# Optimization experiments

Measured on AMD Instinct MI355X. Metric: run time of the kernel, lower is better.

The kernel has to match this reference:

```python
import jax, jax.numpy as jnp
import numpy as np

# --- static config (matches init_kwargs / input_specs) ---
N_GRAPHS = 32
NODES = 1000          # num_nodes per graph
N = N_GRAPHS * NODES  # 32000 total nodes
F_IN = 128            # num_features
E_DIM = 16            # edge_attr_dim
H, C = 4, 16          # heads, GAT_dim
HC = H * C            # 64
E = 512000            # edges (before self-loops)
PROJ = 8              # proj_nodes
OUT = 256             # output_dim
NEG_SLOPE = 0.2       # PyG GATConv default


def setup_inputs() -> dict:
    key = jax.random.key(0)
    ks = jax.random.split(key, 20)
    s = 0.1
    return {
        "x": jax.random.normal(ks[0], (N, F_IN), jnp.float32),
        "edge_attr": jax.random.normal(ks[1], (E, E_DIM), jnp.float32),
        # layer 0 (input_conv): F_IN -> H*C
        "W0":   jax.random.normal(ks[2], (F_IN, HC), jnp.float32) * s,
        "a_s0": jax.random.normal(ks[3], (H, C), jnp.float32) * s,
        "a_d0": jax.random.normal(ks[4], (H, C), jnp.float32) * s,
        "W_e0": jax.random.normal(ks[5], (E_DIM, HC), jnp.float32) * s,
        "a_e0": jax.random.normal(ks[6], (H, C), jnp.float32) * s,
        "b0":   jnp.zeros((HC,), jnp.float32),
        # layers 1..2 stacked: HC -> H*C
        "Wg":   jax.random.normal(ks[7], (2, HC, HC), jnp.float32) * s,
        "a_sg": jax.random.normal(ks[8], (2, H, C), jnp.float32) * s,
        "a_dg": jax.random.normal(ks[9], (2, H, C), jnp.float32) * s,
        "W_eg": jax.random.normal(ks[10], (2, E_DIM, HC), jnp.float32) * s,
        "a_eg": jax.random.normal(ks[11], (2, H, C), jnp.float32) * s,
        "bg":   jnp.zeros((2, HC), jnp.float32),
        # node_proj: HC -> PROJ ; fc_out: NODES*PROJ -> OUT
        "Wp": jax.random.normal(ks[12], (HC, PROJ), jnp.float32) * s,
        "bp": jnp.zeros((PROJ,), jnp.float32),
        "Wo": jax.random.normal(ks[13], (NODES * PROJ, OUT), jnp.float32) * (s / 4),
        "bo": jnp.zeros((OUT,), jnp.float32),
        "edge_index": jax.random.randint(ks[14], (2, E), 0, N, jnp.int32),
        "batch": jnp.repeat(jnp.arange(N_GRAPHS, dtype=jnp.int32), NODES),
    }


def _gat_layer(x, src, dst, eattr, W, a_s, a_d, W_e, a_e, b):
    """PyG GATConv (concat=True, shared src/dst lin, edge_dim) forward."""
    xl = (x @ W).reshape(N, H, C)                       # [N,H,C]
    al_s = jnp.sum(xl * a_s, axis=-1)                   # [N,H]
    al_d = jnp.sum(xl * a_d, axis=-1)                   # [N,H]
    el = (eattr @ W_e).reshape(-1, H, C)                # [Ef,H,C]
    al_e = jnp.sum(el * a_e, axis=-1)                   # [Ef,H]
    logits = jax.nn.leaky_relu(al_s[src] + al_d[dst] + al_e, NEG_SLOPE)
    # segment softmax over destination nodes (every node has a self-loop)
    mx = jax.ops.segment_max(logits, dst, num_segments=N)
    p = jnp.exp(logits - mx[dst])
    denom = jax.ops.segment_sum(p, dst, num_segments=N)
    alpha = p / denom[dst]                               # [Ef,H]
    out = jax.ops.segment_sum(xl[src] * alpha[..., None], dst, num_segments=N)
    return out.reshape(N, HC) + b


def reference(x, edge_attr, W0, a_s0, a_d0, W_e0, a_e0, b0,
              Wg, a_sg, a_dg, W_eg, a_eg, bg,
              Wp, bp, Wo, bo, edge_index, batch):
    src, dst = edge_index[0], edge_index[1]
    # PyG add_self_loops with fill_value='mean': per-dst mean of incoming edge_attr
    deg = jax.ops.segment_sum(jnp.ones((E,), edge_attr.dtype), dst, num_segments=N)
    loop_attr = jax.ops.segment_sum(edge_attr, dst, num_segments=N) / jnp.maximum(deg, 1.0)[:, None]
    loops = jnp.arange(N, dtype=src.dtype)
    src_f = jnp.concatenate([src, loops])
    dst_f = jnp.concatenate([dst, loops])
    ea_f = jnp.concatenate([edge_attr, loop_attr], axis=0)   # [E+N, E_DIM]

    h = jax.nn.relu(_gat_layer(x, src_f, dst_f, ea_f, W0, a_s0, a_d0, W_e0, a_e0, b0))
    for i in range(2):
        h = jax.nn.relu(_gat_layer(h, src_f, dst_f, ea_f,
                                   Wg[i], a_sg[i], a_dg[i], W_eg[i], a_eg[i], bg[i]))
    h = jax.nn.relu(h @ Wp + bp)                             # [N, PROJ]
    B = batch.shape[0] // NODES                              # static batch count
    h = h.reshape(B, NODES * PROJ)
    return h @ Wo + bo                                       # [B, OUT]
```

## Files before the change

kernel.cpp:

```cpp
#include <hip/hip_runtime.h>
#include <hip/hip_bf16.h>
#include <hip/hip_fp16.h>

#define N_NODES 32000
#define FIN     128
#define E_EDGES 512000
#define EF_EDGES 544000
#define HC      64
#define XSTR    72
#define NGRAPH  32
#define PROJ    8
#define OUT_DIM 256

static __device__ inline unsigned short f2bf(float f) {
  unsigned int x = __float_as_uint(f);
  unsigned int r = (x + 0x7fffu + ((x >> 16) & 1u)) >> 16;
  return (unsigned short)r;
}
static __device__ inline float bf2f(unsigned short u) {
  return __uint_as_float((unsigned int)u << 16);
}
static __device__ inline unsigned short f2h(float f) {
  return __half_as_ushort(__float2half(f));
}
static __device__ inline float h2f(unsigned short u) {
  return __half2float(__ushort_as_half(u));
}

__global__ __launch_bounds__(256) void zero_kernel(int* __restrict__ deg) {
  deg[blockIdx.x * 256 + threadIdx.x] = 0;
}

__global__ __launch_bounds__(256) void deg_kernel(const int* __restrict__ ei,
                                                  int* __restrict__ deg) {
  int e = blockIdx.x * 256 + threadIdx.x;
  atomicAdd(&deg[ei[E_EDGES + e]], 1);
}

__global__ __launch_bounds__(256) void scan1_kernel(const int* __restrict__ deg,
                                                    int* __restrict__ offs,
                                                    int* __restrict__ bsum) {
  int idx = blockIdx.x * 256 + threadIdx.x;
  int lane = threadIdx.x & 63;
  int w = threadIdx.x >> 6;
  int v = deg[idx] + 1;
  int s = v;
#pragma unroll
  for (int off = 1; off < 64; off <<= 1) {
    int t = __shfl_up(s, off);
    if (lane >= off) s += t;
  }
  __shared__ int wsum[4];
  if (lane == 63) wsum[w] = s;
  __syncthreads();
  int add = 0;
#pragma unroll
  for (int i = 0; i < 4; ++i) add += (i < w) ? wsum[i] : 0;
  int incl = s + add;
  offs[idx] = incl - v;
  if (threadIdx.x == 255) bsum[blockIdx.x] = incl;
}

__global__ __launch_bounds__(256) void scan3_kernel(const int* __restrict__ bsum,
                                                    int* __restrict__ offs,
                                                    int* __restrict__ nxt) {
  __shared__ int wsum[4];
  int tid = threadIdx.x, bid = blockIdx.x;
  int lane = tid & 63, w = tid >> 6;
  int v = (tid < bid) ? bsum[tid] : 0;
#pragma unroll
  for (int off = 1; off < 64; off <<= 1) v += __shfl_xor(v, off);
  if (lane == 0) wsum[w] = v;
  __syncthreads();
  int boff = wsum[0] + wsum[1] + wsum[2] + wsum[3];
  int idx = bid * 256 + tid;
  int o = offs[idx] + boff;
  offs[idx] = o;
  nxt[idx] = o;
  if (bid == 0 && tid == 0) offs[N_NODES] = EF_EDGES;
}

__global__ __launch_bounds__(256) void fill_kernel(const int* __restrict__ ei,
                                                   int* __restrict__ nxt,
                                                   int* __restrict__ csr_src,
                                                   int* __restrict__ csr_eid) {
  int e = blockIdx.x * 256 + threadIdx.x;
  int s, d;
  if (e < E_EDGES) { s = ei[e]; d = ei[E_EDGES + e]; }
  else             { s = e - E_EDGES; d = s; }
  int pos = atomicAdd(&nxt[d], 1);
  csr_src[pos] = s;
  csr_eid[pos] = e;
}

__device__ __forceinline__ void compute_Me(float (*sMe)[16][4],
                                           const float* __restrict__ W_e0,
                                           const float* __restrict__ a_e0,
                                           const float* __restrict__ W_eg,
                                           const float* __restrict__ a_eg) {
  int tid = threadIdx.x;
  if (tid < 192) {
    int l = tid >> 6, r6 = tid & 63, d = r6 >> 2, h = r6 & 3;
    const float* We = (l == 0) ? W_e0 : W_eg + (size_t)(l - 1) * 16 * HC;
    const float* ae = (l == 0) ? a_e0 : a_eg + (size_t)(l - 1) * 64;
    float s = 0.f;
#pragma unroll
    for (int c = 0; c < 16; ++c) s += We[d * HC + h * 16 + c] * ae[h * 16 + c];
    sMe[l][d][h] = s;
  }
  __syncthreads();
}

__global__ __launch_bounds__(256) void edge_kernel(const float* __restrict__ edge_attr,
                                                   const float* __restrict__ W_e0,
                                                   const float* __restrict__ a_e0,
                                                   const float* __restrict__ W_eg,
                                                   const float* __restrict__ a_eg,
                                                   const int* __restrict__ offs,
                                                   const int* __restrict__ csr_eid,
                                                   unsigned short* __restrict__ lgE) {
  __shared__ float sMe[3][16][4];
  __shared__ float sMean[4][16];
  compute_Me(sMe, W_e0, a_e0, W_eg, a_eg);
  int b = blockIdx.x;
  int tid = threadIdx.x;
  if (b < 8000) {
    int lane = tid & 63, wv = tid >> 6;
    int n = b * 4 + wv;
    int k = lane & 15, g = lane >> 4;
    int beg = offs[n], end = offs[n + 1];
    float s = 0.f;
    int posl = -1;
    for (int i = beg + g; i < end; i += 4) {
      int e = csr_eid[i];
      if (e < E_EDGES) s += edge_attr[(size_t)e * 16 + k];
      else posl = i;
    }
    s += __shfl_xor(s, 16);
    s += __shfl_xor(s, 32);
    posl = max(posl, __shfl_xor(posl, 16));
    posl = max(posl, __shfl_xor(posl, 32));
    int degv = end - beg - 1;
    float mean = s / fmaxf((float)degv, 1.f);
    if (g == 0) sMean[wv][k] = mean;
    if (lane < 3) {
      int l = lane;
      float r0 = 0.f, r1 = 0.f, r2 = 0.f, r3 = 0.f;
#pragma unroll
      for (int d = 0; d < 16; ++d) {
        float a = sMean[wv][d];
        r0 = fmaf(a, sMe[l][d][0], r0);
        r1 = fmaf(a, sMe[l][d][1], r1);
        r2 = fmaf(a, sMe[l][d][2], r2);
        r3 = fmaf(a, sMe[l][d][3], r3);
      }
      unsigned long long u =
          (unsigned long long)f2h(r0) |
          ((unsigned long long)f2h(r1) << 16) |
          ((unsigned long long)f2h(r2) << 32) |
          ((unsigned long long)f2h(r3) << 48);
      *(unsigned long long*)&lgE[((size_t)l * EF_EDGES + posl) * 4] = u;
    }
  } else {
    int pos = (b - 8000) * 256 + tid;
    int e = csr_eid[pos];
    if (e < E_EDGES) {
      float av[16];
      *(float4*)&av[0]  = *(const float4*)&edge_attr[(size_t)e * 16 + 0];
      *(float4*)&av[4]  = *(const float4*)&edge_attr[(size_t)e * 16 + 4];
      *(float4*)&av[8]  = *(const float4*)&edge_attr[(size_t)e * 16 + 8];
      *(float4*)&av[12] = *(const float4*)&edge_attr[(size_t)e * 16 + 12];
#pragma unroll
      for (int l = 0; l < 3; ++l) {
        float r0 = 0.f, r1 = 0.f, r2 = 0.f, r3 = 0.f;
#pragma unroll
        for (int d = 0; d < 16; ++d) {
          float a = av[d];
          r0 = fmaf(a, sMe[l][d][0], r0);
          r1 = fmaf(a, sMe[l][d][1], r1);
          r2 = fmaf(a, sMe[l][d][2], r2);
          r3 = fmaf(a, sMe[l][d][3], r3);
        }
        unsigned long long u =
            (unsigned long long)f2h(r0) |
            ((unsigned long long)f2h(r1) << 16) |
            ((unsigned long long)f2h(r2) << 32) |
            ((unsigned long long)f2h(r3) << 48);
        __builtin_nontemporal_store(
            u, (unsigned long long*)&lgE[((size_t)l * EF_EDGES + pos) * 4]);
      }
    }
  }
}

template <int K>
__global__ __launch_bounds__(256) void transform_kernel(const float* __restrict__ A,
                                                        const float* __restrict__ W,
                                                        const float* __restrict__ a_s,
                                                        const float* __restrict__ a_d,
                                                        unsigned short* __restrict__ xlb,
                                                        float* __restrict__ al_d) {
  __shared__ float sW[64][64];
  __shared__ float sA[64][65];
  int tid = threadIdx.x;
  int row0 = blockIdx.x * 64;
  int tx = tid & 15, ty = tid >> 4;
  int c0 = tx * 4, r0 = ty * 4;
  float acc[4][4] = {};
  for (int kc = 0; kc < K; kc += 64) {
    for (int i = tid; i < 1024; i += 256) {
      int kk = i >> 4, c4 = (i & 15) * 4;
      *(float4*)&sW[kk][c4] = *(const float4*)&W[(size_t)(kc + kk) * HC + c4];
    }
    for (int i = tid; i < 1024; i += 256) {
      int r = i >> 4, k4 = (i & 15) * 4;
      float4 v = *(const float4*)&A[(size_t)(row0 + r) * K + kc + k4];
      sA[r][k4 + 0] = v.x; sA[r][k4 + 1] = v.y;
      sA[r][k4 + 2] = v.z; sA[r][k4 + 3] = v.w;
    }
    __syncthreads();
#pragma unroll 8
    for (int kk = 0; kk < 64; ++kk) {
      float4 w = *(float4*)&sW[kk][c0];
      float a0 = sA[r0 + 0][kk];
      float a1 = sA[r0 + 1][kk];
      float a2 = sA[r0 + 2][kk];
      float a3 = sA[r0 + 3][kk];
      acc[0][0] = fmaf(a0, w.x, acc[0][0]); acc[0][1] = fmaf(a0, w.y, acc[0][1]);
      acc[0][2] = fmaf(a0, w.z, acc[0][2]); acc[0][3] = fmaf(a0, w.w, acc[0][3]);
      acc[1][0] = fmaf(a1, w.x, acc[1][0]); acc[1][1] = fmaf(a1, w.y, acc[1][1]);
      acc[1][2] = fmaf(a1, w.z, acc[1][2]); acc[1][3] = fmaf(a1, w.w, acc[1][3]);
      acc[2][0] = fmaf(a2, w.x, acc[2][0]); acc[2][1] = fmaf(a2, w.y, acc[2][1]);
      acc[2][2] = fmaf(a2, w.z, acc[2][2]); acc[2][3] = fmaf(a2, w.w, acc[2][3]);
      acc[3][0] = fmaf(a3, w.x, acc[3][0]); acc[3][1] = fmaf(a3, w.y, acc[3][1]);
      acc[3][2] = fmaf(a3, w.z, acc[3][2]); acc[3][3] = fmaf(a3, w.w, acc[3][3]);
    }
    __syncthreads();
  }
  float asv[4], adv[4];
#pragma unroll
  for (int j = 0; j < 4; ++j) { asv[j] = a_s[c0 + j]; adv[j] = a_d[c0 + j]; }
  int hd = tx >> 2;
#pragma unroll
  for (int i = 0; i < 4; ++i) {
    int r = row0 + r0 + i;
    ushort4 u = make_ushort4(f2bf(acc[i][0]), f2bf(acc[i][1]),
                             f2bf(acc[i][2]), f2bf(acc[i][3]));
    *(ushort4*)&xlb[(size_t)r * XSTR + c0] = u;
    float ps = acc[i][0] * asv[0] + acc[i][1] * asv[1] + acc[i][2] * asv[2] + acc[i][3] * asv[3];
    float pd = acc[i][0] * adv[0] + acc[i][1] * adv[1] + acc[i][2] * adv[2] + acc[i][3] * adv[3];
    ps += __shfl_xor(ps, 1); ps += __shfl_xor(ps, 2);
    pd += __shfl_xor(pd, 1); pd += __shfl_xor(pd, 2);
    if ((tx & 3) == 0) {
      *(float*)&xlb[(size_t)r * XSTR + 64 + hd * 2] = ps;
      al_d[(size_t)r * 4 + hd] = pd;
    }
  }
}

template <int FUSE_PROJ>
__global__ __launch_bounds__(256, 4) void gather_kernel(const int* __restrict__ offs,
                                                        const int* __restrict__ csr_src,
                                                        const unsigned short* __restrict__ lg,
                                                        const unsigned short* __restrict__ xlb,
                                                        const float* __restrict__ al_d,
                                                        const float* __restrict__ bias,
                                                        const float* __restrict__ Wp,
                                                        const float* __restrict__ bp,
                                                        float* __restrict__ outp) {
  int tid = threadIdx.x;
  int lane = tid & 63;
  int n = blockIdx.x * 4 + (tid >> 6);
  int u = lane & 31;
  int hf = lane >> 5;
  int c0 = u * 2;
  int hd = u >> 3;
  int beg = offs[n], end = offs[n + 1];
  float ald = al_d[(size_t)n * 4 + hd];
  float denom = 0.f, a0 = 0.f, a1 = 0.f;
  for (int ib = beg; ib < end; ib += 16) {
    int sq[8]; unsigned short gq[8]; float pm[8];
#pragma unroll
    for (int q = 0; q < 8; ++q) {
      int j = ib + hf + q * 2;
      bool ok = j < end;
      int jc = ok ? j : beg;
      sq[q] = csr_src[jc];
      gq[q] = lg[(size_t)jc * 4 + hd];
      pm[q] = ok ? 1.f : 0.f;
    }
    unsigned int xq[8]; float alsq[8];
#pragma unroll
    for (int q = 0; q < 8; ++q) {
      const unsigned short* row = &xlb[(size_t)sq[q] * XSTR];
      xq[q] = *(const unsigned int*)&row[c0];
      alsq[q] = *(const float*)&row[64 + hd * 2];
    }
#pragma unroll
    for (int q = 0; q < 8; ++q) {
      float l = h2f(gq[q]) + alsq[q] + ald;
      l = (l > 0.f) ? l : 0.2f * l;
      float p = pm[q] * __expf(l);
      denom += p;
      a0 = fmaf(p, bf2f((unsigned short)(xq[q] & 0xffff)), a0);
      a1 = fmaf(p, bf2f((unsigned short)(xq[q] >> 16)), a1);
    }
  }
  denom += __shfl_xor(denom, 32);
  a0 += __shfl_xor(a0, 32);
  a1 += __shfl_xor(a1, 32);
  float hv0 = fmaxf(a0 / denom + bias[c0], 0.f);
  float hv1 = fmaxf(a1 / denom + bias[c0 + 1], 0.f);
  if constexpr (!FUSE_PROJ) {
    if (hf == 0) {
      float2 o; o.x = hv0; o.y = hv1;
      *(float2*)&outp[(size_t)n * HC + c0] = o;
    }
  } else {
    float pj[8];
#pragma unroll
    for (int j = 0; j < 8; ++j)
      pj[j] = (hf == 0) ? hv0 * Wp[c0 * PROJ + j] + hv1 * Wp[(c0 + 1) * PROJ + j] : 0.f;
#pragma unroll
    for (int off = 1; off < 64; off <<= 1) {
#pragma unroll
      for (int j = 0; j < 8; ++j) pj[j] += __shfl_xor(pj[j], off);
    }
    if (lane < 8) {
      float v = pj[0];
      v = (lane == 1) ? pj[1] : v;
      v = (lane == 2) ? pj[2] : v;
      v = (lane == 3) ? pj[3] : v;
      v = (lane == 4) ? pj[4] : v;
      v = (lane == 5) ? pj[5] : v;
      v = (lane == 6) ? pj[6] : v;
      v = (lane == 7) ? pj[7] : v;
      outp[(size_t)n * PROJ + lane] = fmaxf(v + bp[lane], 0.f);
    }
  }
}

__global__ __launch_bounds__(256) void fc1_kernel(const float* __restrict__ p,
                                                  const float* __restrict__ Wo,
                                                  float* __restrict__ part) {
  __shared__ float sp[NGRAPH][250];
  int kc = blockIdx.x;
  int ct = blockIdx.y;
  int tid = threadIdx.x;
  for (int i = tid; i < NGRAPH * 250; i += 256) {
    int g = i / 250, kk = i % 250;
    sp[g][kk] = p[(size_t)g * 8000 + kc * 250 + kk];
  }
  __syncthreads();
  int c = ct * 64 + (tid & 63);
  int kg = tid >> 6;
  float acc[NGRAPH] = {};
  for (int kk = kg; kk < 250; kk += 4) {
    float w = __builtin_nontemporal_load(&Wo[(size_t)(kc * 250 + kk) * OUT_DIM + c]);
#pragma unroll
    for (int g = 0; g < NGRAPH; ++g) acc[g] = fmaf(sp[g][kk], w, acc[g]);
  }
  int ch = kc * 4 + kg;
#pragma unroll
  for (int g = 0; g < NGRAPH; ++g)
    part[((size_t)ch * NGRAPH + g) * OUT_DIM + c] = acc[g];
}

__global__ __launch_bounds__(256) void fc2_kernel(const float* __restrict__ part,
                                                  const float* __restrict__ bo,
                                                  float* __restrict__ out) {
  int i = blockIdx.x * 256 + threadIdx.x;
  int g = i >> 8, c = i & 255;
  float s = bo[c];
  for (int ch = 0; ch < 128; ++ch) s += part[((size_t)ch * NGRAPH + g) * OUT_DIM + c];
  out[i] = s;
}

extern "C" void kernel_launch(void* const* d_in, const int* in_sizes, int n_in,
                              void* d_out, int out_size, void* d_ws, size_t ws_size,
                              hipStream_t stream) {
  const float* x         = (const float*)d_in[0];
  const float* edge_attr = (const float*)d_in[1];
  const float* W0        = (const float*)d_in[2];
  const float* a_s0      = (const float*)d_in[3];
  const float* a_d0      = (const float*)d_in[4];
  const float* W_e0      = (const float*)d_in[5];
  const float* a_e0      = (const float*)d_in[6];
  const float* b0        = (const float*)d_in[7];
  const float* Wg        = (const float*)d_in[8];
  const float* a_sg      = (const float*)d_in[9];
  const float* a_dg      = (const float*)d_in[10];
  const float* W_eg      = (const float*)d_in[11];
  const float* a_eg      = (const float*)d_in[12];
  const float* bg        = (const float*)d_in[13];
  const float* Wp        = (const float*)d_in[14];
  const float* bp        = (const float*)d_in[15];
  const float* Wo        = (const float*)d_in[16];
  const float* bo        = (const float*)d_in[17];
  const int*   ei        = (const int*)d_in[18];

  char* base = (char*)d_ws;
  size_t off = 0;
  auto alloc = [&](size_t bytes) -> void* {
    void* ptr = base + off;
    off = (off + bytes + 255) & ~(size_t)255;
    return ptr;
  };
  int*            deg     = (int*)alloc((size_t)N_NODES * 4);
  int*            offs    = (int*)alloc((size_t)(N_NODES + 1) * 4);
  int*            nxt     = (int*)alloc((size_t)N_NODES * 4);
  int*            bsum    = (int*)alloc(128 * 4);
  int*            csr_src = (int*)alloc((size_t)EF_EDGES * 4);
  int*            csr_eid = (int*)alloc((size_t)EF_EDGES * 4);
  unsigned short* lgE     = (unsigned short*)alloc((size_t)3 * EF_EDGES * 4 * 2);
  unsigned short* xlb     = (unsigned short*)alloc((size_t)N_NODES * XSTR * 2);
  float*          al_d    = (float*)alloc((size_t)N_NODES * 4 * 4);
  float*          hA      = (float*)alloc((size_t)N_NODES * HC * 4);
  float*          hB      = (float*)alloc((size_t)N_NODES * HC * 4);
  float*          pbuf    = (float*)alloc((size_t)N_NODES * PROJ * 4);
  float*          part    = (float*)alloc((size_t)128 * NGRAPH * OUT_DIM * 4);

  zero_kernel<<<N_NODES / 256, 256, 0, stream>>>(deg);
  deg_kernel<<<E_EDGES / 256, 256, 0, stream>>>(ei, deg);
  scan1_kernel<<<N_NODES / 256, 256, 0, stream>>>(deg, offs, bsum);
  scan3_kernel<<<N_NODES / 256, 256, 0, stream>>>(bsum, offs, nxt);
  fill_kernel<<<EF_EDGES / 256, 256, 0, stream>>>(ei, nxt, csr_src, csr_eid);
  edge_kernel<<<8000 + 2125, 256, 0, stream>>>(edge_attr, W_e0, a_e0, W_eg, a_eg,
                                               offs, csr_eid, lgE);
  transform_kernel<FIN><<<N_NODES / 64, 256, 0, stream>>>(x, W0, a_s0, a_d0, xlb, al_d);

  gather_kernel<0><<<N_NODES / 4, 256, 0, stream>>>(offs, csr_src, lgE, xlb,
                                                    al_d, b0, Wp, bp, hA);
  transform_kernel<HC><<<N_NODES / 64, 256, 0, stream>>>(hA, Wg, a_sg, a_dg, xlb, al_d);
  gather_kernel<0><<<N_NODES / 4, 256, 0, stream>>>(offs, csr_src, lgE + (size_t)EF_EDGES * 4,
                                                    xlb, al_d, bg, Wp, bp, hB);
  transform_kernel<HC><<<N_NODES / 64, 256, 0, stream>>>(hB, Wg + HC * HC, a_sg + 64,
                                                         a_dg + 64, xlb, al_d);
  gather_kernel<1><<<N_NODES / 4, 256, 0, stream>>>(offs, csr_src, lgE + (size_t)2 * EF_EDGES * 4,
                                                    xlb, al_d, bg + 64, Wp, bp, pbuf);

  fc1_kernel<<<dim3(32, 4), 256, 0, stream>>>(pbuf, Wo, part);
  fc2_kernel<<<NGRAPH, 256, 0, stream>>>(part, bo, (float*)d_out);
}
```

Measured before the change: 274.7 us.

## Split node features and edge logits into head halves for gather locality

Node features, source attention scalars and edge logits are stored in two head-half planes (heads 0-1 and heads 2-3). The gather kernel now launches two blocks per four nodes, one per half, so each wave's random-row working set is half as large and more of it can stay in cache. The projection partials from the two halves are summed in fc1, which now also applies the projection bias and relu. The cost is twice as many gather blocks, with the csr_src index loads repeated per half.

```diff
diff --git a/kernel.cpp b/kernel.cpp
--- a/kernel.cpp
+++ b/kernel.cpp
@@ -7,7 +7,6 @@
 #define E_EDGES 512000
 #define EF_EDGES 544000
 #define HC      64
-#define XSTR    72
 #define NGRAPH  32
 #define PROJ    8
 #define OUT_DIM 256
@@ -118,7 +117,7 @@
                                                    const float* __restrict__ a_eg,
                                                    const int* __restrict__ offs,
                                                    const int* __restrict__ csr_eid,
-                                                   unsigned short* __restrict__ lgE) {
+                                                   unsigned short* __restrict__ lgEH) {
   __shared__ float sMe[3][16][4];
   __shared__ float sMean[4][16];
   compute_Me(sMe, W_e0, a_e0, W_eg, a_eg);
@@ -143,23 +142,17 @@
     int degv = end - beg - 1;
     float mean = s / fmaxf((float)degv, 1.f);
     if (g == 0) sMean[wv][k] = mean;
-    if (lane < 3) {
-      int l = lane;
-      float r0 = 0.f, r1 = 0.f, r2 = 0.f, r3 = 0.f;
+    if (lane < 6) {
+      int l = lane >> 1, half = lane & 1;
+      float ra = 0.f, rb = 0.f;
 #pragma unroll
       for (int d = 0; d < 16; ++d) {
         float a = sMean[wv][d];
-        r0 = fmaf(a, sMe[l][d][0], r0);
-        r1 = fmaf(a, sMe[l][d][1], r1);
-        r2 = fmaf(a, sMe[l][d][2], r2);
-        r3 = fmaf(a, sMe[l][d][3], r3);
+        ra = fmaf(a, sMe[l][d][half * 2 + 0], ra);
+        rb = fmaf(a, sMe[l][d][half * 2 + 1], rb);
       }
-      unsigned long long u =
-          (unsigned long long)f2h(r0) |
-          ((unsigned long long)f2h(r1) << 16) |
-          ((unsigned long long)f2h(r2) << 32) |
-          ((unsigned long long)f2h(r3) << 48);
-      *(unsigned long long*)&lgE[((size_t)l * EF_EDGES + posl) * 4] = u;
+      unsigned int u = (unsigned int)f2h(ra) | ((unsigned int)f2h(rb) << 16);
+      *(unsigned int*)&lgEH[(((size_t)l * 2 + half) * EF_EDGES + posl) * 2] = u;
     }
   } else {
     int pos = (b - 8000) * 256 + tid;
@@ -181,13 +174,12 @@
           r2 = fmaf(a, sMe[l][d][2], r2);
           r3 = fmaf(a, sMe[l][d][3], r3);
         }
-        unsigned long long u =
-            (unsigned long long)f2h(r0) |
-            ((unsigned long long)f2h(r1) << 16) |
-            ((unsigned long long)f2h(r2) << 32) |
-            ((unsigned long long)f2h(r3) << 48);
+        unsigned int u0 = (unsigned int)f2h(r0) | ((unsigned int)f2h(r1) << 16);
+        unsigned int u1 = (unsigned int)f2h(r2) | ((unsigned int)f2h(r3) << 16);
         __builtin_nontemporal_store(
-            u, (unsigned long long*)&lgE[((size_t)l * EF_EDGES + pos) * 4]);
+            u0, (unsigned int*)&lgEH[(((size_t)l * 2 + 0) * EF_EDGES + pos) * 2]);
+        __builtin_nontemporal_store(
+            u1, (unsigned int*)&lgEH[(((size_t)l * 2 + 1) * EF_EDGES + pos) * 2]);
       }
     }
   }
@@ -198,7 +190,8 @@
                                                         const float* __restrict__ W,
                                                         const float* __restrict__ a_s,
                                                         const float* __restrict__ a_d,
-                                                        unsigned short* __restrict__ xlb,
+                                                        unsigned short* __restrict__ xlbH,
+                                                        float* __restrict__ al_sh,
                                                         float* __restrict__ al_d) {
   __shared__ float sW[64][64];
   __shared__ float sA[64][65];
@@ -241,63 +234,69 @@
 #pragma unroll
   for (int j = 0; j < 4; ++j) { asv[j] = a_s[c0 + j]; adv[j] = a_d[c0 + j]; }
   int hd = tx >> 2;
+  int half = c0 >> 5, cih = c0 & 31;
 #pragma unroll
   for (int i = 0; i < 4; ++i) {
     int r = row0 + r0 + i;
     ushort4 u = make_ushort4(f2bf(acc[i][0]), f2bf(acc[i][1]),
                              f2bf(acc[i][2]), f2bf(acc[i][3]));
-    *(ushort4*)&xlb[(size_t)r * XSTR + c0] = u;
+    *(ushort4*)&xlbH[((size_t)half * N_NODES + r) * 32 + cih] = u;
     float ps = acc[i][0] * asv[0] + acc[i][1] * asv[1] + acc[i][2] * asv[2] + acc[i][3] * asv[3];
     float pd = acc[i][0] * adv[0] + acc[i][1] * adv[1] + acc[i][2] * adv[2] + acc[i][3] * adv[3];
     ps += __shfl_xor(ps, 1); ps += __shfl_xor(ps, 2);
     pd += __shfl_xor(pd, 1); pd += __shfl_xor(pd, 2);
     if ((tx & 3) == 0) {
-      *(float*)&xlb[(size_t)r * XSTR + 64 + hd * 2] = ps;
+      al_sh[((size_t)(hd >> 1) * N_NODES + r) * 2 + (hd & 1)] = ps;
       al_d[(size_t)r * 4 + hd] = pd;
     }
   }
 }
 
 template <int FUSE_PROJ>
-__global__ __launch_bounds__(256, 4) void gather_kernel(const int* __restrict__ offs,
-                                                        const int* __restrict__ csr_src,
-                                                        const unsigned short* __restrict__ lg,
-                                                        const unsigned short* __restrict__ xlb,
-                                                        const float* __restrict__ al_d,
-                                                        const float* __restrict__ bias,
-                                                        const float* __restrict__ Wp,
-                                                        const float* __restrict__ bp,
-                                                        float* __restrict__ outp) {
+__global__ __launch_bounds__(256) void gather_kernel(const int* __restrict__ offs,
+                                                     const int* __restrict__ csr_src,
+                                                     const unsigned short* __restrict__ lgL,
+                                                     const unsigned short* __restrict__ xlbH,
+                                                     const float* __restrict__ al_sh,
+                                                     const float* __restrict__ al_d,
+                                                     const float* __restrict__ bias,
+                                                     const float* __restrict__ Wp,
+                                                     const float* __restrict__ bp,
+                                                     float* __restrict__ outp) {
   int tid = threadIdx.x;
+  int bid = blockIdx.x;
+  int half = bid & 1;
+  int n = (bid >> 1) * 4 + (tid >> 6);
   int lane = tid & 63;
-  int n = blockIdx.x * 4 + (tid >> 6);
-  int u = lane & 31;
-  int hf = lane >> 5;
-  int c0 = u * 2;
-  int hd = u >> 3;
+  int u16 = lane & 15;
+  int gr = lane >> 4;
+  int c0 = u16 * 2;
+  int hd = u16 >> 3;
+  const unsigned short* lgH = lgL + (size_t)half * EF_EDGES * 2;
+  const unsigned short* xh  = xlbH + (size_t)half * N_NODES * 32;
+  const float* ash          = al_sh + (size_t)half * N_NODES * 2;
   int beg = offs[n], end = offs[n + 1];
-  float ald = al_d[(size_t)n * 4 + hd];
+  float ald = al_d[(size_t)n * 4 + half * 2 + hd];
   float denom = 0.f, a0 = 0.f, a1 = 0.f;
-  for (int ib = beg; ib < end; ib += 16) {
-    int sq[8]; unsigned short gq[8]; float pm[8];
-#pragma unroll
-    for (int q = 0; q < 8; ++q) {
-      int j = ib + hf + q * 2;
+  for (int jb = beg; jb < end; jb += 16) {
+    int sq[4]; unsigned short gq[4]; float pm[4];
+#pragma unroll
+    for (int q = 0; q < 4; ++q) {
+      int j = jb + gr + q * 4;
       bool ok = j < end;
       int jc = ok ? j : beg;
       sq[q] = csr_src[jc];
-      gq[q] = lg[(size_t)jc * 4 + hd];
+      gq[q] = lgH[(size_t)jc * 2 + hd];
       pm[q] = ok ? 1.f : 0.f;
     }
-    unsigned int xq[8]; float alsq[8];
-#pragma unroll
-    for (int q = 0; q < 8; ++q) {
-      const unsigned short* row = &xlb[(size_t)sq[q] * XSTR];
-      xq[q] = *(const unsigned int*)&row[c0];
-      alsq[q] = *(const float*)&row[64 + hd * 2];
-    }
-#pragma unroll
-    for (int q = 0; q < 8; ++q) {
+    unsigned int xq[4]; float alsq[4];
+#pragma unroll
+    for (int q = 0; q < 4; ++q) {
+      xq[q] = *(const unsigned int*)&xh[(size_t)sq[q] * 32 + c0];
+      alsq[q] = ash[(size_t)sq[q] * 2 + hd];
+    }
+#pragma unroll
+    for (int q = 0; q < 4; ++q) {
       float l = h2f(gq[q]) + alsq[q] + ald;
       l = (l > 0.f) ? l : 0.2f * l;
       float p = pm[q] * __expf(l);
@@ -306,21 +305,22 @@
       a1 = fmaf(p, bf2f((unsigned short)(xq[q] >> 16)), a1);
     }
   }
-  denom += __shfl_xor(denom, 32);
-  a0 += __shfl_xor(a0, 32);
-  a1 += __shfl_xor(a1, 32);
-  float hv0 = fmaxf(a0 / denom + bias[c0], 0.f);
-  float hv1 = fmaxf(a1 / denom + bias[c0 + 1], 0.f);
+  denom += __shfl_xor(denom, 16); denom += __shfl_xor(denom, 32);
+  a0 += __shfl_xor(a0, 16); a0 += __shfl_xor(a0, 32);
+  a1 += __shfl_xor(a1, 16); a1 += __shfl_xor(a1, 32);
+  int gc = half * 32 + c0;
+  float hv0 = fmaxf(a0 / denom + bias[gc], 0.f);
+  float hv1 = fmaxf(a1 / denom + bias[gc + 1], 0.f);
   if constexpr (!FUSE_PROJ) {
-    if (hf == 0) {
+    if (gr == 0) {
       float2 o; o.x = hv0; o.y = hv1;
-      *(float2*)&outp[(size_t)n * HC + c0] = o;
+      *(float2*)&outp[(size_t)n * HC + gc] = o;
     }
   } else {
     float pj[8];
 #pragma unroll
     for (int j = 0; j < 8; ++j)
-      pj[j] = (hf == 0) ? hv0 * Wp[c0 * PROJ + j] + hv1 * Wp[(c0 + 1) * PROJ + j] : 0.f;
+      pj[j] = (gr == 0) ? hv0 * Wp[gc * PROJ + j] + hv1 * Wp[(gc + 1) * PROJ + j] : 0.f;
 #pragma unroll
     for (int off = 1; off < 64; off <<= 1) {
 #pragma unroll
@@ -335,21 +335,24 @@
       v = (lane == 5) ? pj[5] : v;
       v = (lane == 6) ? pj[6] : v;
       v = (lane == 7) ? pj[7] : v;
-      outp[(size_t)n * PROJ + lane] = fmaxf(v + bp[lane], 0.f);
-    }
-  }
-}
-
-__global__ __launch_bounds__(256) void fc1_kernel(const float* __restrict__ p,
+      outp[((size_t)half * N_NODES + n) * PROJ + lane] = v;
+    }
+  }
+}
+
+__global__ __launch_bounds__(256) void fc1_kernel(const float* __restrict__ pH,
+                                                  const float* __restrict__ bp,
                                                   const float* __restrict__ Wo,
                                                   float* __restrict__ part) {
   __shared__ float sp[NGRAPH][250];
   int kc = blockIdx.x;
   int ct = blockIdx.y;
   int tid = threadIdx.x;
+  const float* pH1 = pH + (size_t)N_NODES * PROJ;
   for (int i = tid; i < NGRAPH * 250; i += 256) {
     int g = i / 250, kk = i % 250;
-    sp[g][kk] = p[(size_t)g * 8000 + kc * 250 + kk];
+    size_t flat = (size_t)g * 8000 + kc * 250 + kk;
+    sp[g][kk] = fmaxf(pH[flat] + pH1[flat] + bp[flat & 7], 0.f);
   }
   __syncthreads();
   int c = ct * 64 + (tid & 63);
@@ -412,12 +415,13 @@
   int*            bsum    = (int*)alloc(128 * 4);
   int*            csr_src = (int*)alloc((size_t)EF_EDGES * 4);
   int*            csr_eid = (int*)alloc((size_t)EF_EDGES * 4);
-  unsigned short* lgE     = (unsigned short*)alloc((size_t)3 * EF_EDGES * 4 * 2);
-  unsigned short* xlb     = (unsigned short*)alloc((size_t)N_NODES * XSTR * 2);
+  unsigned short* lgEH    = (unsigned short*)alloc((size_t)6 * EF_EDGES * 2 * 2);
+  unsigned short* xlbH    = (unsigned short*)alloc((size_t)2 * N_NODES * 32 * 2);
+  float*          al_sh   = (float*)alloc((size_t)2 * N_NODES * 2 * 4);
   float*          al_d    = (float*)alloc((size_t)N_NODES * 4 * 4);
   float*          hA      = (float*)alloc((size_t)N_NODES * HC * 4);
   float*          hB      = (float*)alloc((size_t)N_NODES * HC * 4);
-  float*          pbuf    = (float*)alloc((size_t)N_NODES * PROJ * 4);
+  float*          pbufH   = (float*)alloc((size_t)2 * N_NODES * PROJ * 4);
   float*          part    = (float*)alloc((size_t)128 * NGRAPH * OUT_DIM * 4);
 
   zero_kernel<<<N_NODES / 256, 256, 0, stream>>>(deg);
@@ -426,19 +430,21 @@
   scan3_kernel<<<N_NODES / 256, 256, 0, stream>>>(bsum, offs, nxt);
   fill_kernel<<<EF_EDGES / 256, 256, 0, stream>>>(ei, nxt, csr_src, csr_eid);
   edge_kernel<<<8000 + 2125, 256, 0, stream>>>(edge_attr, W_e0, a_e0, W_eg, a_eg,
-                                               offs, csr_eid, lgE);
-  transform_kernel<FIN><<<N_NODES / 64, 256, 0, stream>>>(x, W0, a_s0, a_d0, xlb, al_d);
-
-  gather_kernel<0><<<N_NODES / 4, 256, 0, stream>>>(offs, csr_src, lgE, xlb,
-                                                    al_d, b0, Wp, bp, hA);
-  transform_kernel<HC><<<N_NODES / 64, 256, 0, stream>>>(hA, Wg, a_sg, a_dg, xlb, al_d);
-  gather_kernel<0><<<N_NODES / 4, 256, 0, stream>>>(offs, csr_src, lgE + (size_t)EF_EDGES * 4,
-                                                    xlb, al_d, bg, Wp, bp, hB);
+                                               offs, csr_eid, lgEH);
+  transform_kernel<FIN><<<N_NODES / 64, 256, 0, stream>>>(x, W0, a_s0, a_d0,
+                                                          xlbH, al_sh, al_d);
+
+  gather_kernel<0><<<16000, 256, 0, stream>>>(offs, csr_src, lgEH, xlbH,
+                                              al_sh, al_d, b0, Wp, bp, hA);
+  transform_kernel<HC><<<N_NODES / 64, 256, 0, stream>>>(hA, Wg, a_sg, a_dg,
+                                                         xlbH, al_sh, al_d);
+  gather_kernel<0><<<16000, 256, 0, stream>>>(offs, csr_src, lgEH + (size_t)2 * EF_EDGES * 2,
+                                              xlbH, al_sh, al_d, bg, Wp, bp, hB);
   transform_kernel<HC><<<N_NODES / 64, 256, 0, stream>>>(hB, Wg + HC * HC, a_sg + 64,
-                                                         a_dg + 64, xlb, al_d);
-  gather_kernel<1><<<N_NODES / 4, 256, 0, stream>>>(offs, csr_src, lgE + (size_t)2 * EF_EDGES * 4,
-                                                    xlb, al_d, bg + 64, Wp, bp, pbuf);
-
-  fc1_kernel<<<dim3(32, 4), 256, 0, stream>>>(pbuf, Wo, part);
+                                                         a_dg + 64, xlbH, al_sh, al_d);
+  gather_kernel<1><<<16000, 256, 0, stream>>>(offs, csr_src, lgEH + (size_t)4 * EF_EDGES * 2,
+                                              xlbH, al_sh, al_d, bg + 64, Wp, bp, pbufH);
+
+  fc1_kernel<<<dim3(32, 4), 256, 0, stream>>>(pbufH, bp, Wo, part);
   fc2_kernel<<<NGRAPH, 256, 0, stream>>>(part, bo, (float*)d_out);
 }
```

Result: slower. 299.6 us (+9.1%).

## Compute edge attention logits once per edge-head and broadcast via shuffles

Applied to the files above, without the earlier changes.

The gather kernel used to compute each edge's attention logit and exp redundantly in all 8 lanes that share a head. It now assigns one lane per (edge, head) pair for 16 edges at a time, so exp and the logit loads happen once. The probabilities and source indices are then broadcast with wave shuffles to the lanes that accumulate the feature columns. The exchange costs many extra shuffles per batch of edges, and the launch-bounds occupancy hint is dropped.

```diff
diff --git a/kernel.cpp b/kernel.cpp
--- a/kernel.cpp
+++ b/kernel.cpp
@@ -259,60 +259,58 @@
 }
 
 template <int FUSE_PROJ>
-__global__ __launch_bounds__(256, 4) void gather_kernel(const int* __restrict__ offs,
-                                                        const int* __restrict__ csr_src,
-                                                        const unsigned short* __restrict__ lg,
-                                                        const unsigned short* __restrict__ xlb,
-                                                        const float* __restrict__ al_d,
-                                                        const float* __restrict__ bias,
-                                                        const float* __restrict__ Wp,
-                                                        const float* __restrict__ bp,
-                                                        float* __restrict__ outp) {
+__global__ __launch_bounds__(256) void gather_kernel(const int* __restrict__ offs,
+                                                     const int* __restrict__ csr_src,
+                                                     const unsigned short* __restrict__ lg,
+                                                     const unsigned short* __restrict__ xlb,
+                                                     const float* __restrict__ al_d,
+                                                     const float* __restrict__ bias,
+                                                     const float* __restrict__ Wp,
+                                                     const float* __restrict__ bp,
+                                                     float* __restrict__ outp) {
   int tid = threadIdx.x;
   int lane = tid & 63;
   int n = blockIdx.x * 4 + (tid >> 6);
-  int u = lane & 31;
-  int hf = lane >> 5;
-  int c0 = u * 2;
-  int hd = u >> 3;
+  int q16 = lane >> 2, hd4 = lane & 3;
+  int eu = lane >> 5, v = lane & 31;
+  int hdB = v >> 3;
   int beg = offs[n], end = offs[n + 1];
-  float ald = al_d[(size_t)n * 4 + hd];
-  float denom = 0.f, a0 = 0.f, a1 = 0.f;
-  for (int ib = beg; ib < end; ib += 16) {
-    int sq[8]; unsigned short gq[8]; float pm[8];
-#pragma unroll
-    for (int q = 0; q < 8; ++q) {
-      int j = ib + hf + q * 2;
-      bool ok = j < end;
-      int jc = ok ? j : beg;
-      sq[q] = csr_src[jc];
-      gq[q] = lg[(size_t)jc * 4 + hd];
-      pm[q] = ok ? 1.f : 0.f;
-    }
-    unsigned int xq[8]; float alsq[8];
-#pragma unroll
-    for (int q = 0; q < 8; ++q) {
-      const unsigned short* row = &xlb[(size_t)sq[q] * XSTR];
-      xq[q] = *(const unsigned int*)&row[c0];
-      alsq[q] = *(const float*)&row[64 + hd * 2];
-    }
-#pragma unroll
-    for (int q = 0; q < 8; ++q) {
-      float l = h2f(gq[q]) + alsq[q] + ald;
-      l = (l > 0.f) ? l : 0.2f * l;
-      float p = pm[q] * __expf(l);
-      denom += p;
-      a0 = fmaf(p, bf2f((unsigned short)(xq[q] & 0xffff)), a0);
-      a1 = fmaf(p, bf2f((unsigned short)(xq[q] >> 16)), a1);
-    }
-  }
-  denom += __shfl_xor(denom, 32);
+  float ald = al_d[(size_t)n * 4 + hd4];
+  float denq = 0.f, a0 = 0.f, a1 = 0.f;
+  for (int jb = beg; jb < end; jb += 16) {
+    int j = jb + q16;
+    bool ok = j < end;
+    int jc = ok ? j : beg;
+    int sq = csr_src[jc];
+    unsigned short lgv = lg[(size_t)jc * 4 + hd4];
+    const unsigned short* rowA = &xlb[(size_t)sq * XSTR];
+    float als = *(const float*)&rowA[64 + hd4 * 2];
+    float l = h2f(lgv) + als + ald;
+    l = fmaxf(l, 0.2f * l);
+    float p = ok ? __expf(l) : 0.f;
+    denq += p;
+#pragma unroll
+    for (int k = 0; k < 8; ++k) {
+      int e = k * 2 + eu;
+      int se = __shfl(sq, e * 4);
+      float pe = __shfl(p, e * 4 + hdB);
+      unsigned int xx = *(const unsigned int*)&xlb[(size_t)se * XSTR + 2 * v];
+      a0 = fmaf(pe, bf2f((unsigned short)(xx & 0xffff)), a0);
+      a1 = fmaf(pe, bf2f((unsigned short)(xx >> 16)), a1);
+    }
+  }
+  denq += __shfl_xor(denq, 4);
+  denq += __shfl_xor(denq, 8);
+  denq += __shfl_xor(denq, 16);
+  denq += __shfl_xor(denq, 32);
+  float denom = __shfl(denq, hdB);
   a0 += __shfl_xor(a0, 32);
   a1 += __shfl_xor(a1, 32);
+  int c0 = v * 2;
   float hv0 = fmaxf(a0 / denom + bias[c0], 0.f);
   float hv1 = fmaxf(a1 / denom + bias[c0 + 1], 0.f);
   if constexpr (!FUSE_PROJ) {
-    if (hf == 0) {
+    if (eu == 0) {
       float2 o; o.x = hv0; o.y = hv1;
       *(float2*)&outp[(size_t)n * HC + c0] = o;
     }
@@ -320,22 +318,22 @@
     float pj[8];
 #pragma unroll
     for (int j = 0; j < 8; ++j)
-      pj[j] = (hf == 0) ? hv0 * Wp[c0 * PROJ + j] + hv1 * Wp[(c0 + 1) * PROJ + j] : 0.f;
+      pj[j] = (eu == 0) ? hv0 * Wp[c0 * PROJ + j] + hv1 * Wp[(c0 + 1) * PROJ + j] : 0.f;
 #pragma unroll
     for (int off = 1; off < 64; off <<= 1) {
 #pragma unroll
       for (int j = 0; j < 8; ++j) pj[j] += __shfl_xor(pj[j], off);
     }
     if (lane < 8) {
-      float v = pj[0];
-      v = (lane == 1) ? pj[1] : v;
-      v = (lane == 2) ? pj[2] : v;
-      v = (lane == 3) ? pj[3] : v;
-      v = (lane == 4) ? pj[4] : v;
-      v = (lane == 5) ? pj[5] : v;
-      v = (lane == 6) ? pj[6] : v;
-      v = (lane == 7) ? pj[7] : v;
-      outp[(size_t)n * PROJ + lane] = fmaxf(v + bp[lane], 0.f);
+      float val = pj[0];
+      val = (lane == 1) ? pj[1] : val;
+      val = (lane == 2) ? pj[2] : val;
+      val = (lane == 3) ? pj[3] : val;
+      val = (lane == 4) ? pj[4] : val;
+      val = (lane == 5) ? pj[5] : val;
+      val = (lane == 6) ? pj[6] : val;
+      val = (lane == 7) ? pj[7] : val;
+      outp[(size_t)n * PROJ + lane] = fmaxf(val + bp[lane], 0.f);
     }
   }
 }
```

Result: faster. 268.7 us (-2.2%).
